# Kernel optimization log

Hardware: AMD Instinct MI355X
Metric: run time of the kernel (lower is better)

The kernel has to match this reference:

```python
import jax, jax.numpy as jnp
import numpy as np

H, C = 4, 32          # num_heads, hidden_channels
NEG_ATT = 0.2         # GAT attention leaky_relu slope (PyG default)
NEG_ACT = 0.01        # F.leaky_relu default slope applied after each conv


def gat_conv(x_src, x_dst, Wsrc, Wdst, a_src, a_dst, bias, src_idx, dst_idx, n_dst):
    """One bipartite GATConv (add_self_loops=False, concat=True)."""
    hs = (x_src @ Wsrc).reshape(-1, H, C)            # [Ns,H,C]
    hd = (x_dst @ Wdst).reshape(-1, H, C)            # [Nd,H,C]
    a_s = (hs * a_src).sum(-1)                       # [Ns,H]
    a_d = (hd * a_dst).sum(-1)                       # [Nd,H]
    e = jax.nn.leaky_relu(a_s[src_idx] + a_d[dst_idx], NEG_ATT)  # [E,H]
    m = jax.ops.segment_max(e, dst_idx, num_segments=n_dst)      # [Nd,H]
    ex = jnp.exp(e - m[dst_idx])
    denom = jax.ops.segment_sum(ex, dst_idx, num_segments=n_dst)
    alpha = ex / (denom[dst_idx] + 1e-16)            # edge softmax over dst
    msg = hs[src_idx] * alpha[:, :, None]            # [E,H,C]
    out = jax.ops.segment_sum(msg, dst_idx, num_segments=n_dst)  # [Nd,H,C]
    return out.reshape(n_dst, H * C) + bias


def setup_inputs() -> dict:
    key = jax.random.key(0)
    ks = jax.random.split(key, 40)
    it = iter(range(40))
    Nu, Nm, E, D, O = 100000, 20000, 500000, 64, 64
    HC = H * C

    def rn(shape, s=0.1):
        return jax.random.normal(ks[next(it)], shape, jnp.float32) * s

    def ri(n, hi):
        return jax.random.randint(ks[next(it)], (n,), 0, hi)

    return {
        "user_ids": jnp.arange(Nu), "movie_ids": jnp.arange(Nm),
        "um_src": ri(E, Nu), "um_dst": ri(E, Nm),
        "mu_src": ri(E, Nm), "mu_dst": ri(E, Nu),
        "user_emb": rn((Nu, D)), "movie_emb": rn((Nm, D)),
        "l1_um_Wsrc": rn((D, HC)), "l1_um_Wdst": rn((D, HC)),
        "l1_um_asrc": rn((H, C)), "l1_um_adst": rn((H, C)), "l1_um_b": rn((HC,)),
        "l1_mu_Wsrc": rn((D, HC)), "l1_mu_Wdst": rn((D, HC)),
        "l1_mu_asrc": rn((H, C)), "l1_mu_adst": rn((H, C)), "l1_mu_b": rn((HC,)),
        "l2_um_W": rn((HC, HC)), "l2_um_asrc": rn((H, C)), "l2_um_adst": rn((H, C)), "l2_um_b": rn((HC,)),
        "l2_mu_W": rn((HC, HC)), "l2_mu_asrc": rn((H, C)), "l2_mu_adst": rn((H, C)), "l2_mu_b": rn((HC,)),
        "Wo": rn((HC, O)), "bo": rn((O,)),
    }


def reference(user_ids, movie_ids, um_src, um_dst, mu_src, mu_dst,
              user_emb, movie_emb,
              l1_um_Wsrc, l1_um_Wdst, l1_um_asrc, l1_um_adst, l1_um_b,
              l1_mu_Wsrc, l1_mu_Wdst, l1_mu_asrc, l1_mu_adst, l1_mu_b,
              l2_um_W, l2_um_asrc, l2_um_adst, l2_um_b,
              l2_mu_W, l2_mu_asrc, l2_mu_adst, l2_mu_b,
              Wo, bo):
    xu = user_emb[user_ids]
    xm = movie_emb[movie_ids]
    Nu, Nm = xu.shape[0], xm.shape[0]
    # layer 1 (HeteroConv sum: each dst type receives exactly one edge type here)
    hm = gat_conv(xu, xm, l1_um_Wsrc, l1_um_Wdst, l1_um_asrc, l1_um_adst, l1_um_b, um_src, um_dst, Nm)
    hu = gat_conv(xm, xu, l1_mu_Wsrc, l1_mu_Wdst, l1_mu_asrc, l1_mu_adst, l1_mu_b, mu_src, mu_dst, Nu)
    xu = jax.nn.leaky_relu(hu, NEG_ACT)
    xm = jax.nn.leaky_relu(hm, NEG_ACT)
    # layer 2 (non-bipartite in_channels int => shared lin for src and dst)
    hm = gat_conv(xu, xm, l2_um_W, l2_um_W, l2_um_asrc, l2_um_adst, l2_um_b, um_src, um_dst, Nm)
    hu = gat_conv(xm, xu, l2_mu_W, l2_mu_W, l2_mu_asrc, l2_mu_adst, l2_mu_b, mu_src, mu_dst, Nu)
    xu = jax.nn.leaky_relu(hu, NEG_ACT)
    xm = jax.nn.leaky_relu(hm, NEG_ACT)
    out_user = xu @ Wo + bo
    out_movie = xm @ Wo + bo
    return out_user, out_movie, xu, xm
```

## Files before the change

kernel.cpp:

```cpp
#include <hip/hip_runtime.h>
#include <hip/hip_bf16.h>
#include <cstdint>


#define HC 128
#define HH 4
#define NWIN 2

typedef __attribute__((ext_vector_type(8))) short bf16x8;
typedef __attribute__((ext_vector_type(4))) float f32x4;

__device__ __forceinline__ short f2bf(float f) {
    return __builtin_bit_cast(short, __float2bfloat16(f));
}
__device__ __forceinline__ float bf2f(ushort u) {
    return __builtin_bit_cast(float, ((unsigned)u) << 16);
}

struct VT { const float* W[8]; const float* a[8]; float* v[8]; };
__global__ void make_v_all_k(VT t) {
    int gid = blockIdx.x * 256 + threadIdx.x;
    int task, base;
    if (gid < 1024) { task = gid >> 8; base = gid & 255; }
    else if (gid < 3072) { int g = gid - 1024; task = 4 + (g >> 9); base = g & 511; }
    else return;
    int k = base >> 2, h = base & 3;
    int coff = (task & 1) * 4;
    const float* wr = t.W[task] + (size_t)k * HC + h * 32;
    const float* ar = t.a[task] + h * 32;
    float s = 0.f;
    #pragma unroll
    for (int c = 0; c < 32; ++c) s = fmaf(wr[c], ar[c], s);
    t.v[task][k * 8 + coff + h] = s;
}

struct PT { const float* W[5]; const float* V[5]; ushort* Wb[5];
            int K[5]; int Nw[5]; int start[6]; };
__global__ void pack_all_k(PT t) {
    int gid = blockIdx.x * 256 + threadIdx.x;
    if (gid >= t.start[5]) return;
    int task = 0;
    while (gid >= t.start[task + 1]) ++task;
    int loc = gid - t.start[task];
    int K = t.K[task], Nw = t.Nw[task];
    int n = loc / K, k = loc % K;
    float v = 0.f;
    if (n < Nw) v = t.W[task][(size_t)k * Nw + n];
    else if (t.V[task] != nullptr && n < Nw + 8) v = t.V[task][k * 8 + (n - Nw)];
    t.Wb[task][loc] = (ushort)f2bf(v);
}

template <int NT, int MODE, bool ABF, bool HIST>
__global__ __launch_bounds__(256) void gemm_dual_k(
    const void* A0, const int* idx0, const ushort* Wb0, ushort* hsb0,
    ushort* atts0, float* attd0, float* C0, const float* bias0, int M0, int nb0,
    const void* A1, const int* idx1, const ushort* Wb1, ushort* hsb1,
    ushort* atts1, float* attd1, float* C1, const float* bias1, int M1, int nb1,
    int K, int ldc,
    const int* hd0, int* hc0, int Eh0,
    const int* hd1, int* hc1, int Eh1, int* hrank) {
    const void* A; const int* aidx; const ushort* Wb; ushort* hsb;
    ushort* atts; float* attd; float* C; const float* bias; int M, bid;
    int nbg = nb0 + nb1;
    if (HIST && (int)blockIdx.x >= nbg) {
        int base = ((int)blockIdx.x - nbg) * 1024 + threadIdx.x;
        #pragma unroll
        for (int j = 0; j < 4; ++j) {
            int e = base + j * 256;
            if (e < Eh0) hrank[e] = atomicAdd(&hc0[hd0[e]], 1);
            else if (e - Eh0 < Eh1) hrank[e] = atomicAdd(&hc1[hd1[e - Eh0]], 1);
        }
        return;
    }
    if ((int)blockIdx.x < nb0) {
        A = A0; aidx = idx0; Wb = Wb0; hsb = hsb0; atts = atts0; attd = attd0;
        C = C0; bias = bias0; M = M0; bid = blockIdx.x;
    } else {
        A = A1; aidx = idx1; Wb = Wb1; hsb = hsb1; atts = atts1; attd = attd1;
        C = C1; bias = bias1; M = M1; bid = blockIdx.x - nb0;
    }
    int lane = threadIdx.x & 63;
    int wave = threadIdx.x >> 6;
    int m_base = bid * 128 + wave * 32;
    int lm = lane & 15;
    int kg = lane >> 4;

    int r0 = m_base + lm, r1 = r0 + 16;
    int cr0 = r0 < M ? r0 : M - 1;
    int cr1 = r1 < M ? r1 : M - 1;
    int row0 = aidx ? aidx[cr0] : cr0;
    int row1 = aidx ? aidx[cr1] : cr1;
    const ushort* bp = Wb + (size_t)lm * K + kg * 8;

    f32x4 acc[2][NT] = {};
    for (int k0 = 0; k0 < K; k0 += 32) {
        bf16x8 a[2];
        if (ABF) {
            const ushort* a0p = (const ushort*)A + (size_t)row0 * K + kg * 8;
            const ushort* a1p = (const ushort*)A + (size_t)row1 * K + kg * 8;
            a[0] = *reinterpret_cast<const bf16x8*>(a0p + k0);
            a[1] = *reinterpret_cast<const bf16x8*>(a1p + k0);
        } else {
            const float* a0p = (const float*)A + (size_t)row0 * K + kg * 8;
            const float* a1p = (const float*)A + (size_t)row1 * K + kg * 8;
            float af[2][8];
            *reinterpret_cast<float4*>(&af[0][0]) = *reinterpret_cast<const float4*>(a0p + k0);
            *reinterpret_cast<float4*>(&af[0][4]) = *reinterpret_cast<const float4*>(a0p + k0 + 4);
            *reinterpret_cast<float4*>(&af[1][0]) = *reinterpret_cast<const float4*>(a1p + k0);
            *reinterpret_cast<float4*>(&af[1][4]) = *reinterpret_cast<const float4*>(a1p + k0 + 4);
            #pragma unroll
            for (int mi = 0; mi < 2; ++mi)
                #pragma unroll
                for (int j = 0; j < 8; ++j) a[mi][j] = f2bf(af[mi][j]);
        }
        #pragma unroll
        for (int nt = 0; nt < NT; ++nt) {
            bf16x8 b = *reinterpret_cast<const bf16x8*>(bp + (size_t)nt * 16 * K + k0);
            acc[0][nt] = __builtin_amdgcn_mfma_f32_16x16x32_bf16(a[0], b, acc[0][nt], 0, 0, 0);
            acc[1][nt] = __builtin_amdgcn_mfma_f32_16x16x32_bf16(a[1], b, acc[1][nt], 0, 0, 0);
        }
    }
    #pragma unroll
    for (int mi = 0; mi < 2; ++mi) {
        int rowb = m_base + mi * 16 + kg * 4;
        if (MODE == 0) {
            #pragma unroll
            for (int nt = 0; nt < NT - 1; ++nt) {
                int col = nt * 16 + lm;
                #pragma unroll
                for (int r = 0; r < 4; ++r) {
                    int row = rowb + r;
                    if (row < M) hsb[(size_t)row * HC + col] = (ushort)f2bf(acc[mi][nt][r]);
                }
            }
            #pragma unroll
            for (int r = 0; r < 4; ++r) {
                int row = rowb + r;
                if (row < M) {
                    float v = acc[mi][NT - 1][r];
                    if (lm < 4) atts[(size_t)row * 4 + lm] = (ushort)f2bf(v);
                    else if (lm < 8) attd[(size_t)row * 4 + (lm - 4)] = v;
                }
            }
        } else {
            #pragma unroll
            for (int nt = 0; nt < NT; ++nt) {
                int col = nt * 16 + lm;
                float bv = bias[col];
                #pragma unroll
                for (int r = 0; r < 4; ++r) {
                    int row = rowb + r;
                    if (row < M) C[(size_t)row * ldc + col] = acc[mi][nt][r] + bv;
                }
            }
        }
    }
}

__device__ __forceinline__ void scan_block_body(
    const int* deg, int n, int len, int* out, int* partial, int b) {
    __shared__ int s[256];
    int i = b * 256 + threadIdx.x;
    int v = (i < n) ? deg[i] : 0;
    s[threadIdx.x] = v;
    __syncthreads();
    for (int off = 1; off < 256; off <<= 1) {
        int t = (threadIdx.x >= off) ? s[threadIdx.x - off] : 0;
        __syncthreads();
        s[threadIdx.x] += t;
        __syncthreads();
    }
    if (i < len) out[i] = s[threadIdx.x] - v;
    if (threadIdx.x == 255) partial[b] = s[255];
}

__global__ void scan_block_dual_k(const int* dM, int nM, int* rsM, int* pM, int nbM,
                                  const int* dU, int nU, int* rsU, int* pU) {
    if ((int)blockIdx.x < nbM)
        scan_block_body(dM, nM, nM + 1, rsM, pM, blockIdx.x);
    else
        scan_block_body(dU, nU, nU + 1, rsU, pU, blockIdx.x - nbM);
}

__global__ void scan_partial_dual_k(int* pM, int nbM, int* pU, int nbU) {
    __shared__ int s[512];
    int t = threadIdx.x;
    for (int seg = 0; seg < 2; ++seg) {
        int* p = seg ? pU : pM;
        int nb = seg ? nbU : nbM;
        int v = (t < nb) ? p[t] : 0;
        s[t] = v;
        __syncthreads();
        for (int off = 1; off < 512; off <<= 1) {
            int x = (t >= off) ? s[t - off] : 0;
            __syncthreads();
            s[t] += x;
            __syncthreads();
        }
        if (t < nb) p[t] = s[t] - v;
        __syncthreads();
    }
}

__global__ void add_off_dual_k(int* __restrict__ oM, const int* __restrict__ pM,
                               int lenM, int nbM,
                               int* __restrict__ oU, const int* __restrict__ pU,
                               int lenU) {
    int b = blockIdx.x;
    if (b < nbM) {
        int i = b * 256 + threadIdx.x;
        if (i < lenM) oM[i] += pM[b];
    } else {
        b -= nbM;
        int i = b * 256 + threadIdx.x;
        if (i < lenU) oU[i] += pU[b];
    }
}

__global__ void fill_dual_k(const int* __restrict__ s0, const int* __restrict__ d0,
                            const int* __restrict__ rs0, int* __restrict__ csr0,
                            int E0, int n0,
                            const int* __restrict__ s1, const int* __restrict__ d1,
                            const int* __restrict__ rs1, int* __restrict__ csr1,
                            int E1, int n1,
                            const int* __restrict__ rank) {
    int e = blockIdx.x * 256 + threadIdx.x;
    int w = blockIdx.y;
    if (e < E0) {
        int d = d0[e];
        int lo = (int)((long)w * n0 / NWIN), hi = (int)((long)(w + 1) * n0 / NWIN);
        if (d >= lo && d < hi) csr0[rs0[d] + rank[e]] = s0[e];
    } else if (e - E0 < E1) {
        int e1 = e - E0;
        int d = d1[e1];
        int lo = (int)((long)w * n1 / NWIN), hi = (int)((long)(w + 1) * n1 / NWIN);
        if (d >= lo && d < hi) csr1[rs1[d] + rank[e]] = s1[e1];
    }
}

template <bool WF32, bool WBF>
__global__ __launch_bounds__(256) void agg16_dual_k(
    const int* __restrict__ rs0, const int* __restrict__ csr0,
    const ushort* __restrict__ hsb0, const ushort* __restrict__ atts0,
    const float* __restrict__ attd0, const float* __restrict__ bias0,
    float* __restrict__ out0, ushort* __restrict__ outb0, int n0,
    const int* __restrict__ rs1, const int* __restrict__ csr1,
    const ushort* __restrict__ hsb1, const ushort* __restrict__ atts1,
    const float* __restrict__ attd1, const float* __restrict__ bias1,
    float* __restrict__ out1, ushort* __restrict__ outb1, int n1) {
    int g = (int)((blockIdx.x * 256u + threadIdx.x) >> 4);
    const int* rs; const int* csr; const ushort* hsb; const ushort* atts;
    const float* attd; const float* bias; float* out; ushort* outb; int node;
    if (g < n0) {
        rs = rs0; csr = csr0; hsb = hsb0; atts = atts0; attd = attd0;
        bias = bias0; out = out0; outb = outb0; node = g;
    } else {
        node = g - n0;
        if (node >= n1) return;
        rs = rs1; csr = csr1; hsb = hsb1; atts = atts1; attd = attd1;
        bias = bias1; out = out1; outb = outb1;
    }
    int c = threadIdx.x & 15;
    int h = c >> 2;
    float ad = attd[node * 4 + h];
    int s0 = rs[node], s1 = rs[node + 1];
    float acc[8] = {};
    float wsum = 0.f;
    int i = s0;
    for (; i + 4 <= s1; i += 4) {
        int sx[4];
        #pragma unroll
        for (int j = 0; j < 4; ++j) sx[j] = csr[i + j];
        bf16x8 hv[4]; float el[4];
        #pragma unroll
        for (int j = 0; j < 4; ++j) {
            hv[j] = *reinterpret_cast<const bf16x8*>(hsb + (size_t)sx[j] * HC + 8 * c);
            el[j] = bf2f(atts[(size_t)sx[j] * 4 + h]);
        }
        #pragma unroll
        for (int j = 0; j < 4; ++j) {
            float e = el[j] + ad;
            e = e > 0.f ? e : 0.2f * e;
            float w = __expf(e);
            wsum += w;
            #pragma unroll
            for (int k = 0; k < 8; ++k)
                acc[k] = fmaf(w, bf2f((ushort)hv[j][k]), acc[k]);
        }
    }
    for (; i < s1; ++i) {
        int src = csr[i];
        bf16x8 hv = *reinterpret_cast<const bf16x8*>(hsb + (size_t)src * HC + 8 * c);
        float e = bf2f(atts[(size_t)src * 4 + h]) + ad;
        e = e > 0.f ? e : 0.2f * e;
        float w = __expf(e);
        wsum += w;
        #pragma unroll
        for (int k = 0; k < 8; ++k)
            acc[k] = fmaf(w, bf2f((ushort)hv[k]), acc[k]);
    }
    float inv = 1.f / (wsum + 1e-16f);
    float v[8];
    #pragma unroll
    for (int k = 0; k < 8; ++k) {
        v[k] = fmaf(acc[k], inv, bias[8 * c + k]);
        v[k] = v[k] > 0.f ? v[k] : 0.01f * v[k];
    }
    if (WF32) {
        float4 o0 = make_float4(v[0], v[1], v[2], v[3]);
        float4 o1 = make_float4(v[4], v[5], v[6], v[7]);
        reinterpret_cast<float4*>(out + (size_t)node * HC + 8 * c)[0] = o0;
        reinterpret_cast<float4*>(out + (size_t)node * HC + 8 * c)[1] = o1;
    }
    if (WBF) {
        bf16x8 u;
        #pragma unroll
        for (int k = 0; k < 8; ++k) u[k] = f2bf(v[k]);
        *reinterpret_cast<bf16x8*>(outb + (size_t)node * HC + 8 * c) = u;
    }
}

extern "C" void kernel_launch(void* const* d_in, const int* in_sizes, int n_in,
                              void* d_out, int out_size, void* d_ws, size_t ws_size,
                              hipStream_t stream) {
    const int Nu = in_sizes[0];
    const int Nm = in_sizes[1];
    const int E1 = in_sizes[2];
    const int E2 = in_sizes[4];
    const int D  = in_sizes[6] / Nu;
    const int O  = in_sizes[27];

    const int*   user_ids  = (const int*)d_in[0];
    const int*   movie_ids = (const int*)d_in[1];
    const int*   um_src    = (const int*)d_in[2];
    const int*   um_dst    = (const int*)d_in[3];
    const int*   mu_src    = (const int*)d_in[4];
    const int*   mu_dst    = (const int*)d_in[5];
    const float* user_emb  = (const float*)d_in[6];
    const float* movie_emb = (const float*)d_in[7];
    const float* l1_um_Wsrc = (const float*)d_in[8];
    const float* l1_um_Wdst = (const float*)d_in[9];
    const float* l1_um_asrc = (const float*)d_in[10];
    const float* l1_um_adst = (const float*)d_in[11];
    const float* l1_um_b    = (const float*)d_in[12];
    const float* l1_mu_Wsrc = (const float*)d_in[13];
    const float* l1_mu_Wdst = (const float*)d_in[14];
    const float* l1_mu_asrc = (const float*)d_in[15];
    const float* l1_mu_adst = (const float*)d_in[16];
    const float* l1_mu_b    = (const float*)d_in[17];
    const float* l2_um_W    = (const float*)d_in[18];
    const float* l2_um_asrc = (const float*)d_in[19];
    const float* l2_um_adst = (const float*)d_in[20];
    const float* l2_um_b    = (const float*)d_in[21];
    const float* l2_mu_W    = (const float*)d_in[22];
    const float* l2_mu_asrc = (const float*)d_in[23];
    const float* l2_mu_adst = (const float*)d_in[24];
    const float* l2_mu_b    = (const float*)d_in[25];
    const float* Wo         = (const float*)d_in[26];
    const float* bo         = (const float*)d_in[27];

    char* p = (char*)d_ws;
    auto alloc = [&](size_t bytes) { void* r = p; p += (bytes + 255) & ~(size_t)255; return r; };
    ushort* hs_u = (ushort*)alloc((size_t)Nu * HC * 2);
    ushort* hs_m = (ushort*)alloc((size_t)Nm * HC * 2);
    ushort* XUb  = (ushort*)alloc((size_t)Nu * HC * 2);
    ushort* XMb  = (ushort*)alloc((size_t)Nm * HC * 2);
    ushort* atts_u = (ushort*)alloc((size_t)Nu * 4 * 2);
    ushort* atts_m = (ushort*)alloc((size_t)Nm * 4 * 2);
    float* attd_u = (float*)alloc((size_t)Nu * 4 * 4);
    float* attd_m = (float*)alloc((size_t)Nm * 4 * 4);
    float* V_u1  = (float*)alloc((size_t)HC * 8 * 4);
    float* V_m1  = (float*)alloc((size_t)HC * 8 * 4);
    float* V_u2  = (float*)alloc((size_t)HC * 8 * 4);
    float* V_m2  = (float*)alloc((size_t)HC * 8 * 4);
    ushort* Wb_u1 = (ushort*)alloc((size_t)144 * D * 2);
    ushort* Wb_m1 = (ushort*)alloc((size_t)144 * D * 2);
    ushort* Wb_u2 = (ushort*)alloc((size_t)144 * HC * 2);
    ushort* Wb_m2 = (ushort*)alloc((size_t)144 * HC * 2);
    ushort* Wb_o  = (ushort*)alloc((size_t)64 * HC * 2);
    int* um_rs  = (int*)alloc((size_t)(Nm + 1) * 4);
    int* mu_rs  = (int*)alloc((size_t)(Nu + 1) * 4);
    int* cnts   = (int*)alloc((size_t)(Nm + Nu) * 4);
    int* um_cnt = cnts;
    int* mu_cnt = cnts + Nm;
    int* um_csr = (int*)alloc((size_t)E1 * 4);
    int* mu_csr = (int*)alloc((size_t)E2 * 4);
    int* rank   = (int*)alloc((size_t)(E1 + E2) * 4);
    int* partM  = (int*)alloc(512 * 4);
    int* partU  = (int*)alloc(512 * 4);

    auto cdiv = [](int a, int b) { return (a + b - 1) / b; };

    {
        VT vt;
        const float* Ws[8] = {l1_um_Wsrc, l1_mu_Wdst, l1_mu_Wsrc, l1_um_Wdst,
                              l2_um_W, l2_mu_W, l2_mu_W, l2_um_W};
        const float* as[8] = {l1_um_asrc, l1_mu_adst, l1_mu_asrc, l1_um_adst,
                              l2_um_asrc, l2_mu_adst, l2_mu_asrc, l2_um_adst};
        float* vs[8] = {V_u1, V_u1, V_m1, V_m1, V_u2, V_u2, V_m2, V_m2};
        for (int i = 0; i < 8; ++i) { vt.W[i] = Ws[i]; vt.a[i] = as[i]; vt.v[i] = vs[i]; }
        make_v_all_k<<<12, 256, 0, stream>>>(vt);

        PT pt;
        const float* pW[5] = {l1_um_Wsrc, l1_mu_Wsrc, l2_um_W, l2_mu_W, Wo};
        const float* pV[5] = {V_u1, V_m1, V_u2, V_m2, nullptr};
        ushort* pB[5] = {Wb_u1, Wb_m1, Wb_u2, Wb_m2, Wb_o};
        int pK[5] = {D, D, HC, HC, HC};
        int pN[5] = {HC, HC, HC, HC, 64};
        int cum = 0;
        for (int i = 0; i < 5; ++i) {
            pt.W[i] = pW[i]; pt.V[i] = pV[i]; pt.Wb[i] = pB[i];
            pt.K[i] = pK[i]; pt.Nw[i] = pN[i];
            pt.start[i] = cum;
            cum += (i < 4 ? 144 : 64) * pK[i];
        }
        pt.start[5] = cum;
        pack_all_k<<<cdiv(cum, 256), 256, 0, stream>>>(pt);
    }

    hipMemsetAsync(cnts, 0, (size_t)(Nm + Nu) * 4, stream);

    float* OU = (float*)d_out;
    float* OM = OU + (size_t)Nu * O;
    float* XU = OM + (size_t)Nm * O;
    float* XM = XU + (size_t)Nu * HC;

    int gbU = cdiv(Nu, 128), gbM = cdiv(Nm, 128);
    int aggBlocks = cdiv((Nm + Nu) * 16, 256);
    int histBlocks = cdiv(E1 + E2, 1024);

    gemm_dual_k<9, 0, false, true><<<gbU + gbM + histBlocks, 256, 0, stream>>>(
        user_emb, user_ids, Wb_u1, hs_u, atts_u, attd_u, nullptr, nullptr, Nu, gbU,
        movie_emb, movie_ids, Wb_m1, hs_m, atts_m, attd_m, nullptr, nullptr, Nm, gbM,
        D, 0,
        um_dst, um_cnt, E1, mu_dst, mu_cnt, E2, rank);

    int nbM = cdiv(Nm + 1, 256), nbU = cdiv(Nu + 1, 256);
    scan_block_dual_k<<<nbM + nbU, 256, 0, stream>>>(um_cnt, Nm, um_rs, partM, nbM,
                                                     mu_cnt, Nu, mu_rs, partU);
    scan_partial_dual_k<<<1, 512, 0, stream>>>(partM, nbM, partU, nbU);
    add_off_dual_k<<<nbM + nbU, 256, 0, stream>>>(um_rs, partM, Nm + 1, nbM,
                                                  mu_rs, partU, Nu + 1);
    {
        dim3 g(cdiv(E1 + E2, 256), NWIN);
        fill_dual_k<<<g, 256, 0, stream>>>(
            um_src, um_dst, um_rs, um_csr, E1, Nm,
            mu_src, mu_dst, mu_rs, mu_csr, E2, Nu, rank);
    }

    agg16_dual_k<false, true><<<aggBlocks, 256, 0, stream>>>(
        um_rs, um_csr, hs_u, atts_u, attd_m, l1_um_b, nullptr, XMb, Nm,
        mu_rs, mu_csr, hs_m, atts_m, attd_u, l1_mu_b, nullptr, XUb, Nu);

    gemm_dual_k<9, 0, true, false><<<gbU + gbM, 256, 0, stream>>>(
        XUb, nullptr, Wb_u2, hs_u, atts_u, attd_u, nullptr, nullptr, Nu, gbU,
        XMb, nullptr, Wb_m2, hs_m, atts_m, attd_m, nullptr, nullptr, Nm, gbM,
        HC, 0,
        nullptr, nullptr, 0, nullptr, nullptr, 0, nullptr);
    agg16_dual_k<true, false><<<aggBlocks, 256, 0, stream>>>(
        um_rs, um_csr, hs_u, atts_u, attd_m, l2_um_b, XM, nullptr, Nm,
        mu_rs, mu_csr, hs_m, atts_m, attd_u, l2_mu_b, XU, nullptr, Nu);

    gemm_dual_k<4, 1, false, false><<<gbU + gbM, 256, 0, stream>>>(
        XU, nullptr, Wb_o, nullptr, nullptr, nullptr, OU, bo, Nu, gbU,
        XM, nullptr, Wb_o, nullptr, nullptr, nullptr, OM, bo, Nm, gbM,
        HC, O,
        nullptr, nullptr, 0, nullptr, nullptr, 0, nullptr);
}
```

Before: 245.1 us.

## Pad degree counters and spread histogram work across GEMM blocks

The degree-count array is padded so each node's counter sits 64 bytes apart (CPAD=16), aiming to reduce atomic contention from counters sharing a cache line. Instead of dedicated histogram blocks appended to the fused GEMM launch, every GEMM block first handles a contiguous slice of edges before doing its tile work. The cost is a 16x larger counter buffer and memset, strided reads in the scan, and GEMM work that now waits behind the atomics in every block.

```diff
diff --git a/kernel.cpp b/kernel.cpp
--- a/kernel.cpp
+++ b/kernel.cpp
@@ -6,6 +6,7 @@
 #define HC 128
 #define HH 4
 #define NWIN 2
+#define CPAD 16
 
 typedef __attribute__((ext_vector_type(8))) short bf16x8;
 typedef __attribute__((ext_vector_type(4))) float f32x4;
@@ -59,19 +60,21 @@
     int K, int ldc,
     const int* hd0, int* hc0, int Eh0,
     const int* hd1, int* hc1, int Eh1, int* hrank) {
+    if (HIST) {
+        int nbg = nb0 + nb1;
+        int totE = Eh0 + Eh1;
+        int epb = (totE + nbg - 1) / nbg;
+        int e0 = (int)blockIdx.x * epb;
+        int e1 = min(e0 + epb, totE);
+        for (int e = e0 + (int)threadIdx.x; e < e1; e += 256) {
+            int r;
+            if (e < Eh0) r = atomicAdd(&hc0[(size_t)hd0[e] * CPAD], 1);
+            else r = atomicAdd(&hc1[(size_t)hd1[e - Eh0] * CPAD], 1);
+            hrank[e] = r;
+        }
+    }
     const void* A; const int* aidx; const ushort* Wb; ushort* hsb;
     ushort* atts; float* attd; float* C; const float* bias; int M, bid;
-    int nbg = nb0 + nb1;
-    if (HIST && (int)blockIdx.x >= nbg) {
-        int base = ((int)blockIdx.x - nbg) * 1024 + threadIdx.x;
-        #pragma unroll
-        for (int j = 0; j < 4; ++j) {
-            int e = base + j * 256;
-            if (e < Eh0) hrank[e] = atomicAdd(&hc0[hd0[e]], 1);
-            else if (e - Eh0 < Eh1) hrank[e] = atomicAdd(&hc1[hd1[e - Eh0]], 1);
-        }
-        return;
-    }
     if ((int)blockIdx.x < nb0) {
         A = A0; aidx = idx0; Wb = Wb0; hsb = hsb0; atts = atts0; attd = attd0;
         C = C0; bias = bias0; M = M0; bid = blockIdx.x;
@@ -161,7 +164,7 @@
     const int* deg, int n, int len, int* out, int* partial, int b) {
     __shared__ int s[256];
     int i = b * 256 + threadIdx.x;
-    int v = (i < n) ? deg[i] : 0;
+    int v = (i < n) ? deg[(size_t)i * CPAD] : 0;
     s[threadIdx.x] = v;
     __syncthreads();
     for (int off = 1; off < 256; off <<= 1) {
@@ -380,9 +383,9 @@
     ushort* Wb_o  = (ushort*)alloc((size_t)64 * HC * 2);
     int* um_rs  = (int*)alloc((size_t)(Nm + 1) * 4);
     int* mu_rs  = (int*)alloc((size_t)(Nu + 1) * 4);
-    int* cnts   = (int*)alloc((size_t)(Nm + Nu) * 4);
+    int* cnts   = (int*)alloc((size_t)(Nm + Nu) * CPAD * 4);
     int* um_cnt = cnts;
-    int* mu_cnt = cnts + Nm;
+    int* mu_cnt = cnts + (size_t)Nm * CPAD;
     int* um_csr = (int*)alloc((size_t)E1 * 4);
     int* mu_csr = (int*)alloc((size_t)E2 * 4);
     int* rank   = (int*)alloc((size_t)(E1 + E2) * 4);
@@ -418,7 +421,7 @@
         pack_all_k<<<cdiv(cum, 256), 256, 0, stream>>>(pt);
     }
 
-    hipMemsetAsync(cnts, 0, (size_t)(Nm + Nu) * 4, stream);
+    hipMemsetAsync(cnts, 0, (size_t)(Nm + Nu) * CPAD * 4, stream);
 
     float* OU = (float*)d_out;
     float* OM = OU + (size_t)Nu * O;
@@ -427,9 +430,8 @@
 
     int gbU = cdiv(Nu, 128), gbM = cdiv(Nm, 128);
     int aggBlocks = cdiv((Nm + Nu) * 16, 256);
-    int histBlocks = cdiv(E1 + E2, 1024);
-
-    gemm_dual_k<9, 0, false, true><<<gbU + gbM + histBlocks, 256, 0, stream>>>(
+
+    gemm_dual_k<9, 0, false, true><<<gbU + gbM, 256, 0, stream>>>(
         user_emb, user_ids, Wb_u1, hs_u, atts_u, attd_u, nullptr, nullptr, Nu, gbU,
         movie_emb, movie_ids, Wb_m1, hs_m, atts_m, attd_m, nullptr, nullptr, Nm, gbM,
         D, 0,
```

Result: faster. 236.7 us (-3.4%).
